# Kernel optimization log

Hardware: AMD Instinct MI355X
Metric: run time of the kernel (lower is better)

The kernel has to match this reference:

```python
import jax, jax.numpy as jnp
import numpy as np

C = 1.0        # curvature parameter (manifold curvature -1/C)
EPS = 1e-7


def expmap0_space(v, k):
    # v: [..., ds] spatial tangent vector at the hyperboloid origin (time comp 0)
    # returns ambient point [..., ds+1] = (sqrt(k)cosh(|v|/sqrt(k)), sqrt(k)sinh(|v|/sqrt(k)) v/|v|)
    sk = jnp.sqrt(k)
    n = jnp.maximum(jnp.linalg.norm(v, axis=-1, keepdims=True), EPS)
    t = sk * jnp.cosh(n / sk)
    s = sk * jnp.sinh(n / sk) * (v / n)
    return jnp.concatenate([t, s], axis=-1)


def logmap0_space(p, k):
    # p: [..., ds+1] hyperboloid point -> spatial tangent [..., ds] at origin
    sk = jnp.sqrt(k)
    t, s = p[..., :1], p[..., 1:]
    ns = jnp.maximum(jnp.linalg.norm(s, axis=-1, keepdims=True), EPS)
    d = sk * jnp.arccosh(jnp.maximum(t / sk, 1.0 + EPS))
    return d * (s / ns)


def setup_inputs() -> dict:
    key = jax.random.key(0)
    N, DS, E = 50000, 127, 800000
    ks = jax.random.split(key, 8)
    x = jax.random.normal(ks[0], (N, DS), dtype=jnp.float32) * 0.1
    edge_src = jax.random.randint(ks[1], (E,), 0, N)
    edge_dst = jax.random.randint(ks[2], (E,), 0, N)
    edge_weight = jax.random.uniform(ks[3], (E,), dtype=jnp.float32) / 16.0  # ~1/deg norm
    sc = 1.0 / np.sqrt(DS)
    W1 = jax.random.normal(ks[4], (DS, DS), dtype=jnp.float32) * sc
    b1 = jnp.zeros((DS,), dtype=jnp.float32)
    W2 = jax.random.normal(ks[5], (DS, DS), dtype=jnp.float32) * sc
    b2 = jnp.zeros((DS,), dtype=jnp.float32)
    return {"x": x, "W1": W1, "b1": b1, "W2": W2, "b2": b2,
            "edge_src": edge_src, "edge_dst": edge_dst, "edge_weight": edge_weight}


def reference(x, W1, b1, W2, b2, edge_src, edge_dst, edge_weight):
    N = x.shape[0]
    # encode(): cat zero time column + expmap0 onto hyperboloid
    p = expmap0_space(x, C)                 # [N, ds+1]
    h = logmap0_space(p, C)                 # tangent features at origin [N, ds]
    for (W, b) in ((W1, b1), (W2, b2)):
        # hyperbolic linear in tangent space
        z = h @ W + b                       # [N, ds]
        # adjacency-based neighbor aggregation (sparse spmm via edge list)
        msg = edge_weight[:, None] * z[edge_src]          # [E, ds] irregular gather
        agg = jax.ops.segment_sum(msg, edge_dst, num_segments=N)
        # activation + skip connection, back onto the manifold between layers
        h = jax.nn.relu(agg) + h
        h = logmap0_space(expmap0_space(h, C), C)
    return expmap0_space(h, C)              # [N, ds+1] on hyperboloid
```

## Files before the change

kernel.cpp:

```cpp
#include <hip/hip_runtime.h>

#define EPS 1e-7f
#define DS 127
#define DP 128
#define NBMAX 512
#define CAP 4096
#define CH 2048
#define PADB ((DP * DP + DP + 255) / 256)
#define BM 64

typedef short bf16x8 __attribute__((ext_vector_type(8)));
typedef float f32x4  __attribute__((ext_vector_type(4)));
typedef float f32x2  __attribute__((ext_vector_type(2)));

__device__ __forceinline__ float wave_sum(float v) {
#pragma unroll
    for (int off = 32; off > 0; off >>= 1)
        v += __shfl_xor(v, off, 64);
    return v;
}

__device__ __forceinline__ int wave_sum_i(int v) {
#pragma unroll
    for (int off = 32; off > 0; off >>= 1)
        v += __shfl_xor(v, off, 64);
    return v;
}

__device__ __forceinline__ unsigned short f2bf(float f) {
    unsigned u = __float_as_uint(f);
    unsigned r = (u + 0x7FFFu + ((u >> 16) & 1u)) >> 16;
    return (unsigned short)r;
}

__device__ __forceinline__ unsigned pack_bf2(float a, float b) {
    return (unsigned)f2bf(a) | ((unsigned)f2bf(b) << 16);
}

__device__ __forceinline__ unsigned char f2fp8(float v) {
    return (unsigned char)(__builtin_amdgcn_cvt_pk_fp8_f32(v, v, 0, false) & 0xFF);
}

__device__ __forceinline__ float logexp_scale(float n2) {
    float nrm = sqrtf(n2);
    return (nrm >= 4.472136e-4f) ? 1.0f : (4.472136e-4f / fmaxf(nrm, EPS));
}

__device__ __forceinline__ void sinhcosh(float n, float& sh, float& ch) {
    float e  = __expf(n);
    float em = __expf(-n);
    sh = 0.5f * (e - em);
    ch = 0.5f * (e + em);
}

__device__ __forceinline__ void padT_dev(int pb, int tid,
        const float* __restrict__ W, const float* __restrict__ b,
        unsigned short* __restrict__ Wt, float* __restrict__ bp) {
    int i = pb * 256 + tid;
    if (i < DP * DP) {
        int n = i >> 7, k = i & (DP - 1);
        Wt[i] = (k < DS && n < DS) ? f2bf(W[k * DS + n]) : (unsigned short)0;
    } else if (i < DP * DP + DP) {
        int j = i - DP * DP;
        bp[j] = (j < DS) ? b[j] : 0.f;
    }
}

__device__ void binA_dev(int abid, int tid,
        const int* __restrict__ es, const int* __restrict__ ed,
        const float* __restrict__ ew,
        int* __restrict__ gcnt, unsigned* __restrict__ stg_pk,
        unsigned char* __restrict__ stg_r, int E) {
    __shared__ int  lcnt[NBMAX];
    __shared__ int  loff[NBMAX];
    __shared__ int  gbase[NBMAX];
    __shared__ unsigned       lst_pk[CH];
    __shared__ unsigned short lst_d[CH];

    int lane = tid & 63;
    int base = abid * CH;
    int cnt  = min(CH, E - base);

    for (int b = tid; b < NBMAX; b += 256) lcnt[b] = 0;
    __syncthreads();

    unsigned pk[CH / 256];
    int      rd[CH / 256];
#pragma unroll
    for (int k = 0; k < CH / 256; k++) {
        int i = base + k * 256 + tid;
        if (i < E) {
            int d = ed[i];
            rd[k] = d;
            pk[k] = ((unsigned)f2bf(ew[i]) << 16) | (unsigned)es[i];
            atomicAdd(&lcnt[d >> 7], 1);
        } else {
            rd[k] = -1;
        }
    }
    __syncthreads();

    if (tid < 64) {
        int carry = 0;
        for (int c = 0; c < NBMAX; c += 64) {
            int v = lcnt[c + lane];
            int inc = v;
#pragma unroll
            for (int off = 1; off < 64; off <<= 1) {
                int t = __shfl_up(inc, off, 64);
                if (lane >= off) inc += t;
            }
            loff[c + lane] = carry + inc - v;
            carry += __shfl(inc, 63, 64);
        }
    }
    __syncthreads();
    for (int b = tid; b < NBMAX; b += 256) lcnt[b] = 0;
    __syncthreads();

#pragma unroll
    for (int k = 0; k < CH / 256; k++) {
        if (rd[k] >= 0) {
            int b = rd[k] >> 7;
            int slot = loff[b] + atomicAdd(&lcnt[b], 1);
            lst_pk[slot] = pk[k];
            lst_d[slot]  = (unsigned short)rd[k];
        }
    }
    __syncthreads();

    for (int b = tid; b < NBMAX; b += 256) {
        int c = lcnt[b];
        gbase[b] = c ? atomicAdd(&gcnt[b], c) : 0;
    }
    __syncthreads();

    for (int s = tid; s < cnt; s += 256) {
        unsigned p = lst_pk[s];
        int d = lst_d[s];
        int b = d >> 7;
        int idx = gbase[b] + (s - loff[b]);
        if (idx >= CAP) idx = CAP - 1;
        stg_pk[(size_t)b * CAP + idx] = p;
        stg_r [(size_t)b * CAP + idx] = (unsigned char)(d & 127);
    }
}

__device__ void binB_dev(int b, int tid,
        const unsigned* __restrict__ stg_pk, const unsigned char* __restrict__ stg_r,
        const int* __restrict__ gcnt,
        int* __restrict__ row_start, unsigned* __restrict__ epk,
        int N, int E) {
    __shared__ int rcnt[128];
    __shared__ int roff[128];
    __shared__ int sh_bb;

    int lane = tid & 63;
    int wave = tid >> 6;
    int cnt  = min(gcnt[b], CAP);
    const unsigned*      in_pk = stg_pk + (size_t)b * CAP;
    const unsigned char* in_r  = stg_r  + (size_t)b * CAP;

    if (tid < 128) rcnt[tid] = 0;
    if (b == 0 && tid == 0) row_start[N] = E;
    __syncthreads();

    if (wave == 3) {
        int acc = 0;
        for (int c = lane; c < b; c += 64) acc += min(gcnt[c], CAP);
        acc = wave_sum_i(acc);
        if (lane == 0) sh_bb = acc;
    } else {
        for (int i = tid; i < cnt; i += 192)
            atomicAdd(&rcnt[in_r[i]], 1);
    }
    __syncthreads();
    int bb = sh_bb;

    if (tid < 64) {
        int carry = 0;
        for (int c = 0; c < 128; c += 64) {
            int v = rcnt[c + lane];
            int inc = v;
#pragma unroll
            for (int off = 1; off < 64; off <<= 1) {
                int t = __shfl_up(inc, off, 64);
                if (lane >= off) inc += t;
            }
            roff[c + lane] = carry + inc - v;
            carry += __shfl(inc, 63, 64);
        }
    }
    __syncthreads();

    if (tid < 128) {
        int row = b * 128 + tid;
        if (row < N) row_start[row] = bb + roff[tid];
        rcnt[tid] = 0;
    }
    __syncthreads();

    for (int i = tid; i < cnt; i += 256) {
        int r = in_r[i];
        int pos = atomicAdd(&rcnt[r], 1);
        epk[bb + roff[r] + pos] = in_pk[i];
    }
}

__global__ __launch_bounds__(256) void k1_kernel(
        const int* __restrict__ es, const int* __restrict__ ed,
        const float* __restrict__ ew,
        int* __restrict__ gcnt, unsigned* __restrict__ stg_pk,
        unsigned char* __restrict__ stg_r, int E,
        const float* __restrict__ W1, const float* __restrict__ b1,
        unsigned short* __restrict__ Wt1, float* __restrict__ bp1,
        const float* __restrict__ W2, const float* __restrict__ b2,
        unsigned short* __restrict__ Wt2, float* __restrict__ bp2, int nA) {
    int bid = blockIdx.x;
    int tid = threadIdx.x;
    if (bid < nA) {
        binA_dev(bid, tid, es, ed, ew, gcnt, stg_pk, stg_r, E);
        return;
    }
    bid -= nA;
    int layer = (bid >= PADB);
    int pb    = bid - layer * PADB;
    padT_dev(pb, tid, layer ? W2 : W1, layer ? b2 : b1,
             layer ? Wt2 : Wt1, layer ? bp2 : bp1);
}

__device__ void fgemm_dev(int gbid, int tid,
        const float* __restrict__ x, unsigned* __restrict__ hbu,
        const unsigned short* __restrict__ Wt, const float* __restrict__ bp,
        unsigned char* __restrict__ z8, int N) {
    __shared__ unsigned sha[64 * 64];

    int wave = tid >> 6;
    int lane = tid & 63;
    int r0   = gbid * BM;

    f32x2 xv[16];
#pragma unroll
    for (int r = 0; r < 16; r++) {
        int row = r0 + wave * 16 + r;
        if (row < N) {
            const float* rp = x + (size_t)row * DS;
            xv[r].x = rp[2 * lane];
            xv[r].y = (lane < 63) ? rp[2 * lane + 1] : 0.f;
        } else {
            xv[r].x = 0.f; xv[r].y = 0.f;
        }
    }
#pragma unroll
    for (int r = 0; r < 16; r++) {
        int lr  = wave * 16 + r;
        int row = r0 + lr;
        float s = logexp_scale(wave_sum(xv[r].x * xv[r].x + xv[r].y * xv[r].y));
        unsigned pk = pack_bf2(s * xv[r].x, (lane < 63) ? s * xv[r].y : 0.f);
        sha[lr * 64 + lane] = pk;
        if (row < N) hbu[(size_t)row * (DP / 2) + lane] = pk;
    }

    int m    = lane & 15;
    int quad = lane >> 4;

    f32x4 acc[8];
#pragma unroll
    for (int t = 0; t < 8; t++) acc[t] = (f32x4){0.f, 0.f, 0.f, 0.f};

    const unsigned* shrow = sha + (size_t)(wave * 16 + m) * 64;
    bf16x8 a[4];
#pragma unroll
    for (int kq = 0; kq < 4; kq++)
        a[kq] = *(const bf16x8*)(shrow + kq * 16 + quad * 4);

#pragma unroll
    for (int kq = 0; kq < 4; kq++) {
#pragma unroll
        for (int nt = 0; nt < 8; nt++) {
            bf16x8 bfr = ((const bf16x8*)(Wt + (size_t)(nt * 16 + m) * DP))[kq * 4 + quad];
            acc[nt] = __builtin_amdgcn_mfma_f32_16x16x32_bf16(a[kq], bfr, acc[nt], 0, 0, 0);
        }
    }

    int rw0 = r0 + wave * 16;
#pragma unroll
    for (int nt = 0; nt < 8; nt++) {
        float bias = bp[nt * 16 + m];
#pragma unroll
        for (int reg = 0; reg < 4; reg++) {
            int row = rw0 + quad * 4 + reg;
            if (row < N)
                z8[(size_t)row * DP + nt * 16 + m] = f2fp8(acc[nt][reg] + bias);
        }
    }
}

__global__ __launch_bounds__(256) void k2_kernel(
        const unsigned* __restrict__ stg_pk, const unsigned char* __restrict__ stg_r,
        const int* __restrict__ gcnt,
        int* __restrict__ row_start, unsigned* __restrict__ epk,
        const float* __restrict__ x, unsigned* __restrict__ hbu,
        const unsigned short* __restrict__ Wt, const float* __restrict__ bp,
        unsigned char* __restrict__ z8, int N, int E, int nB) {
    int bid = blockIdx.x;
    int tid = threadIdx.x;
    if (bid < nB) {
        binB_dev(bid, tid, stg_pk, stg_r, gcnt, row_start, epk, N, E);
        return;
    }
    fgemm_dev(bid - nB, tid, x, hbu, Wt, bp, z8, N);
}

__global__ __launch_bounds__(256) void gemm_kernel(
        const unsigned short* __restrict__ hb,
        const unsigned short* __restrict__ Wt,
        const float* __restrict__ bp,
        unsigned char* __restrict__ z8, int N) {
    int wave = threadIdx.x >> 6;
    int lane = threadIdx.x & 63;
    int m    = lane & 15;
    int quad = lane >> 4;
    int r0   = blockIdx.x * BM + wave * 16;

    f32x4 acc[8];
#pragma unroll
    for (int t = 0; t < 8; t++) acc[t] = (f32x4){0.f, 0.f, 0.f, 0.f};

    const bf16x8* arow = (const bf16x8*)(hb + (size_t)(r0 + m) * DP);
    bf16x8 a[4];
#pragma unroll
    for (int kq = 0; kq < 4; kq++) a[kq] = arow[kq * 4 + quad];

#pragma unroll
    for (int kq = 0; kq < 4; kq++) {
#pragma unroll
        for (int nt = 0; nt < 8; nt++) {
            bf16x8 bfr = ((const bf16x8*)(Wt + (size_t)(nt * 16 + m) * DP))[kq * 4 + quad];
            acc[nt] = __builtin_amdgcn_mfma_f32_16x16x32_bf16(a[kq], bfr, acc[nt], 0, 0, 0);
        }
    }

#pragma unroll
    for (int nt = 0; nt < 8; nt++) {
        float bias = bp[nt * 16 + m];
#pragma unroll
        for (int reg = 0; reg < 4; reg++) {
            int row = r0 + quad * 4 + reg;
            if (row < N)
                z8[(size_t)row * DP + nt * 16 + m] = f2fp8(acc[nt][reg] + bias);
        }
    }
}

__device__ __forceinline__ void agg_round32(
        const unsigned char* __restrict__ zc, const unsigned* __restrict__ epk,
        int e, int end, bool lo, int q4, float* A) {
    unsigned p[32];
#pragma unroll
    for (int i = 0; i < 32; i++) {
        unsigned v = epk[e + i];
        p[i] = (e + i < end) ? v : 0u;
    }
    unsigned ud[16];
#pragma unroll
    for (int i = 0; i < 16; i++) {
        unsigned sel = lo ? p[2 * i] : p[2 * i + 1];
        ud[i] = *(const unsigned*)(zc + (((size_t)(sel & 0xFFFFu)) << 7) + q4);
    }
#pragma unroll
    for (int i = 0; i < 16; i++) {
        unsigned sel = lo ? p[2 * i] : p[2 * i + 1];
        float wf = __uint_as_float(sel & 0xFFFF0000u);
        f32x2 zl = __builtin_amdgcn_cvt_pk_f32_fp8(ud[i], false);
        f32x2 zh = __builtin_amdgcn_cvt_pk_f32_fp8(ud[i], true);
        A[0] = fmaf(wf, zl.x, A[0]);
        A[1] = fmaf(wf, zl.y, A[1]);
        A[2] = fmaf(wf, zh.x, A[2]);
        A[3] = fmaf(wf, zh.y, A[3]);
    }
}

__device__ __forceinline__ void agg_round32_pair(
        const unsigned char* __restrict__ zc, const unsigned* __restrict__ epk,
        int e0, int end0, int e1, int end1, bool lo, int q4,
        float* A, float* B) {
    unsigned p0[32], p1[32];
#pragma unroll
    for (int i = 0; i < 32; i++) {
        unsigned v = epk[e0 + i];
        p0[i] = (e0 + i < end0) ? v : 0u;
    }
#pragma unroll
    for (int i = 0; i < 32; i++) {
        unsigned v = epk[e1 + i];
        p1[i] = (e1 + i < end1) ? v : 0u;
    }
    unsigned ud0[16], ud1[16];
#pragma unroll
    for (int i = 0; i < 16; i++) {
        unsigned sel = lo ? p0[2 * i] : p0[2 * i + 1];
        ud0[i] = *(const unsigned*)(zc + (((size_t)(sel & 0xFFFFu)) << 7) + q4);
    }
#pragma unroll
    for (int i = 0; i < 16; i++) {
        unsigned sel = lo ? p1[2 * i] : p1[2 * i + 1];
        ud1[i] = *(const unsigned*)(zc + (((size_t)(sel & 0xFFFFu)) << 7) + q4);
    }
#pragma unroll
    for (int i = 0; i < 16; i++) {
        unsigned sel = lo ? p0[2 * i] : p0[2 * i + 1];
        float wf = __uint_as_float(sel & 0xFFFF0000u);
        f32x2 zl = __builtin_amdgcn_cvt_pk_f32_fp8(ud0[i], false);
        f32x2 zh = __builtin_amdgcn_cvt_pk_f32_fp8(ud0[i], true);
        A[0] = fmaf(wf, zl.x, A[0]);
        A[1] = fmaf(wf, zl.y, A[1]);
        A[2] = fmaf(wf, zh.x, A[2]);
        A[3] = fmaf(wf, zh.y, A[3]);
    }
#pragma unroll
    for (int i = 0; i < 16; i++) {
        unsigned sel = lo ? p1[2 * i] : p1[2 * i + 1];
        float wf = __uint_as_float(sel & 0xFFFF0000u);
        f32x2 zl = __builtin_amdgcn_cvt_pk_f32_fp8(ud1[i], false);
        f32x2 zh = __builtin_amdgcn_cvt_pk_f32_fp8(ud1[i], true);
        B[0] = fmaf(wf, zl.x, B[0]);
        B[1] = fmaf(wf, zl.y, B[1]);
        B[2] = fmaf(wf, zh.x, B[2]);
        B[3] = fmaf(wf, zh.y, B[3]);
    }
}

template <bool LAST>
__global__ __launch_bounds__(256) void agg_f_tpl(
                          const unsigned char* __restrict__ zc,
                          const unsigned* __restrict__ hbu_in,
                          const int* __restrict__ row_start,
                          const unsigned* __restrict__ epk,
                          unsigned* __restrict__ hbu_out,
                          float* __restrict__ out, int N) {
    int wid  = (int)((blockIdx.x * blockDim.x + threadIdx.x) >> 6);
    int lane = threadIdx.x & 63;
    int gw0  = wid * 2;
    if (gw0 >= N) return;
    gw0 = __builtin_amdgcn_readfirstlane(gw0);
    bool lo = (lane < 32);
    int  q  = lane & 31;
    int  q4 = q << 2;
    bool has1 = (gw0 + 1 < N);

    int rs0 = row_start[gw0];
    int rs1 = row_start[gw0 + 1];
    int rs2 = has1 ? row_start[gw0 + 2] : rs1;

    uint2 hu0 = *(const uint2*)(hbu_in + (size_t)gw0 * (DP / 2) + 2 * q);
    uint2 hu1 = has1 ? *(const uint2*)(hbu_in + (size_t)(gw0 + 1) * (DP / 2) + 2 * q)
                     : make_uint2(0u, 0u);

    float A[4] = {0.f, 0.f, 0.f, 0.f};
    float B[4] = {0.f, 0.f, 0.f, 0.f};

    agg_round32_pair(zc, epk, rs0, rs1, rs1, rs2, lo, q4, A, B);
    int e0 = rs0 + 32, e1 = rs1 + 32;
    while (e0 < rs1) { agg_round32(zc, epk, e0, rs1, lo, q4, A); e0 += 32; }
    while (e1 < rs2) { agg_round32(zc, epk, e1, rs2, lo, q4, B); e1 += 32; }

#pragma unroll
    for (int k = 0; k < 4; k++) {
        A[k] += __shfl_xor(A[k], 32, 64);
        B[k] += __shfl_xor(B[k], 32, 64);
    }

    unsigned hx[2][2] = {{hu0.x, hu0.y}, {hu1.x, hu1.y}};
#pragma unroll
    for (int r = 0; r < 2; r++) {
        if (r == 1 && !has1) break;
        int gw = gw0 + r;
        const float* Ac = (r == 0) ? A : B;
        float x0 = __uint_as_float(hx[r][0] << 16)          + fmaxf(Ac[0], 0.f);
        float x1 = __uint_as_float(hx[r][0] & 0xFFFF0000u)  + fmaxf(Ac[1], 0.f);
        float x2 = __uint_as_float(hx[r][1] << 16)          + fmaxf(Ac[2], 0.f);
        float x3 = __uint_as_float(hx[r][1] & 0xFFFF0000u)  + fmaxf(Ac[3], 0.f);

        float n2 = x0 * x0 + x1 * x1 + x2 * x2 + x3 * x3;
#pragma unroll
        for (int off = 16; off > 0; off >>= 1)
            n2 += __shfl_xor(n2, off, 64);

        float scale = logexp_scale(n2);
        float y0 = scale * x0, y1 = scale * x1;
        float y2 = scale * x2, y3 = scale * x3;

        if (!LAST) {
            unsigned* orow = hbu_out + (size_t)gw * (DP / 2);
            if (lo) orow[2 * q]     = pack_bf2(y0, y1);
            else    orow[2 * q + 1] = pack_bf2(y2, y3);
        } else {
            float ny = fmaxf(scale * sqrtf(n2), EPS);
            float shy, chy;
            sinhcosh(ny, shy, chy);
            float sc = shy / ny;
            float* orow = out + (size_t)gw * DP;
            if (lane == 0) orow[0] = chy;
            if (lo) {
                orow[1 + 4 * q] = sc * y0;
                orow[2 + 4 * q] = sc * y1;
            } else {
                orow[3 + 4 * q] = sc * y2;
                if (q < 31) orow[4 + 4 * q] = sc * y3;
            }
        }
    }
}

extern "C" void kernel_launch(void* const* d_in, const int* in_sizes, int n_in,
                              void* d_out, int out_size, void* d_ws, size_t ws_size,
                              hipStream_t stream) {
    const float* x  = (const float*)d_in[0];
    const float* W1 = (const float*)d_in[1];
    const float* b1 = (const float*)d_in[2];
    const float* W2 = (const float*)d_in[3];
    const float* b2 = (const float*)d_in[4];
    const int*   es = (const int*)d_in[5];
    const int*   ed = (const int*)d_in[6];
    const float* ew = (const float*)d_in[7];

    const int N  = in_sizes[0] / DS;
    const int E  = in_sizes[5];
    const int NR = (N + BM - 1) / BM * BM;
    const int NB = (N + 127) >> 7;

    unsigned short* hb  = (unsigned short*)d_ws;
    unsigned char*  z8  = (unsigned char*)(hb + (size_t)NR * DP);
    unsigned short* Wt1 = (unsigned short*)(z8 + (size_t)N * DP);
    unsigned short* Wt2 = Wt1 + DP * DP;
    float* bp1          = (float*)(Wt2 + DP * DP);
    float* bp2          = bp1 + DP;
    unsigned* epk       = (unsigned*)(bp2 + DP);
    int*   row_start    = (int*)(epk + E);
    int*   gcnt         = row_start + N + 1;
    unsigned* stg_pk    = (unsigned*)(gcnt + NBMAX);
    unsigned char* stg_r = (unsigned char*)(stg_pk + (size_t)NBMAX * CAP);

    unsigned* hbu = (unsigned*)hb;

    const int gemmBlocks = (N + BM - 1) / BM;
    const int binABlocks = (E + CH - 1) / CH;
    const int aggWaves   = (N + 1) / 2;
    const int aggBlocks  = (aggWaves + 3) / 4;

    hipMemsetAsync(gcnt, 0, NBMAX * sizeof(int), stream);

    k1_kernel<<<binABlocks + 2 * PADB, 256, 0, stream>>>(
        es, ed, ew, gcnt, stg_pk, stg_r, E,
        W1, b1, Wt1, bp1, W2, b2, Wt2, bp2, binABlocks);

    k2_kernel<<<NB + gemmBlocks, 256, 0, stream>>>(
        stg_pk, stg_r, gcnt, row_start, epk,
        x, hbu, Wt1, bp1, z8, N, E, NB);

    agg_f_tpl<false><<<aggBlocks, 256, 0, stream>>>(z8, hbu, row_start, epk,
                                                    hbu, nullptr, N);

    gemm_kernel<<<gemmBlocks, 256, 0, stream>>>(hb, Wt2, bp2, z8, N);

    agg_f_tpl<true><<<aggBlocks, 256, 0, stream>>>(z8, hbu, row_start, epk,
                                                   nullptr, (float*)d_out, N);
}
```

Before: 222.1 us.

## Make aggregation kernel persistent with grid-stride rows, one row per wave

Replaces the two-rows-per-wave aggregation with a persistent grid-stride loop. A fixed grid of 2048 blocks is launched with an occupancy hint of 8 blocks per CU, and each wave handles one destination row at a time. The bf16 output store is merged into a single 64-bit write from the lower half-wave, and the final fp32 row is likewise written only by the lower half. This cuts launch and tail imbalance and register pressure, at the cost of fewer independent gathers in flight per wave than the paired-row version had.

```diff
diff --git a/kernel.cpp b/kernel.cpp
--- a/kernel.cpp
+++ b/kernel.cpp
@@ -353,7 +353,7 @@
     }
 }
 
-__device__ __forceinline__ void agg_round32(
+__device__ __forceinline__ void agg_win32(
         const unsigned char* __restrict__ zc, const unsigned* __restrict__ epk,
         int e, int end, bool lo, int q4, float* A) {
     unsigned p[32];
@@ -381,106 +381,40 @@
     }
 }
 
-__device__ __forceinline__ void agg_round32_pair(
-        const unsigned char* __restrict__ zc, const unsigned* __restrict__ epk,
-        int e0, int end0, int e1, int end1, bool lo, int q4,
-        float* A, float* B) {
-    unsigned p0[32], p1[32];
-#pragma unroll
-    for (int i = 0; i < 32; i++) {
-        unsigned v = epk[e0 + i];
-        p0[i] = (e0 + i < end0) ? v : 0u;
-    }
-#pragma unroll
-    for (int i = 0; i < 32; i++) {
-        unsigned v = epk[e1 + i];
-        p1[i] = (e1 + i < end1) ? v : 0u;
-    }
-    unsigned ud0[16], ud1[16];
-#pragma unroll
-    for (int i = 0; i < 16; i++) {
-        unsigned sel = lo ? p0[2 * i] : p0[2 * i + 1];
-        ud0[i] = *(const unsigned*)(zc + (((size_t)(sel & 0xFFFFu)) << 7) + q4);
-    }
-#pragma unroll
-    for (int i = 0; i < 16; i++) {
-        unsigned sel = lo ? p1[2 * i] : p1[2 * i + 1];
-        ud1[i] = *(const unsigned*)(zc + (((size_t)(sel & 0xFFFFu)) << 7) + q4);
-    }
-#pragma unroll
-    for (int i = 0; i < 16; i++) {
-        unsigned sel = lo ? p0[2 * i] : p0[2 * i + 1];
-        float wf = __uint_as_float(sel & 0xFFFF0000u);
-        f32x2 zl = __builtin_amdgcn_cvt_pk_f32_fp8(ud0[i], false);
-        f32x2 zh = __builtin_amdgcn_cvt_pk_f32_fp8(ud0[i], true);
-        A[0] = fmaf(wf, zl.x, A[0]);
-        A[1] = fmaf(wf, zl.y, A[1]);
-        A[2] = fmaf(wf, zh.x, A[2]);
-        A[3] = fmaf(wf, zh.y, A[3]);
-    }
-#pragma unroll
-    for (int i = 0; i < 16; i++) {
-        unsigned sel = lo ? p1[2 * i] : p1[2 * i + 1];
-        float wf = __uint_as_float(sel & 0xFFFF0000u);
-        f32x2 zl = __builtin_amdgcn_cvt_pk_f32_fp8(ud1[i], false);
-        f32x2 zh = __builtin_amdgcn_cvt_pk_f32_fp8(ud1[i], true);
-        B[0] = fmaf(wf, zl.x, B[0]);
-        B[1] = fmaf(wf, zl.y, B[1]);
-        B[2] = fmaf(wf, zh.x, B[2]);
-        B[3] = fmaf(wf, zh.y, B[3]);
-    }
-}
-
 template <bool LAST>
-__global__ __launch_bounds__(256) void agg_f_tpl(
+__global__ __launch_bounds__(256, 8) void agg_f_tpl(
                           const unsigned char* __restrict__ zc,
                           const unsigned* __restrict__ hbu_in,
                           const int* __restrict__ row_start,
                           const unsigned* __restrict__ epk,
                           unsigned* __restrict__ hbu_out,
-                          float* __restrict__ out, int N) {
-    int wid  = (int)((blockIdx.x * blockDim.x + threadIdx.x) >> 6);
+                          float* __restrict__ out, int N, int W) {
+    int gwave = (int)((blockIdx.x * blockDim.x + threadIdx.x) >> 6);
+    gwave = __builtin_amdgcn_readfirstlane(gwave);
     int lane = threadIdx.x & 63;
-    int gw0  = wid * 2;
-    if (gw0 >= N) return;
-    gw0 = __builtin_amdgcn_readfirstlane(gw0);
     bool lo = (lane < 32);
     int  q  = lane & 31;
     int  q4 = q << 2;
-    bool has1 = (gw0 + 1 < N);
-
-    int rs0 = row_start[gw0];
-    int rs1 = row_start[gw0 + 1];
-    int rs2 = has1 ? row_start[gw0 + 2] : rs1;
-
-    uint2 hu0 = *(const uint2*)(hbu_in + (size_t)gw0 * (DP / 2) + 2 * q);
-    uint2 hu1 = has1 ? *(const uint2*)(hbu_in + (size_t)(gw0 + 1) * (DP / 2) + 2 * q)
-                     : make_uint2(0u, 0u);
-
-    float A[4] = {0.f, 0.f, 0.f, 0.f};
-    float B[4] = {0.f, 0.f, 0.f, 0.f};
-
-    agg_round32_pair(zc, epk, rs0, rs1, rs1, rs2, lo, q4, A, B);
-    int e0 = rs0 + 32, e1 = rs1 + 32;
-    while (e0 < rs1) { agg_round32(zc, epk, e0, rs1, lo, q4, A); e0 += 32; }
-    while (e1 < rs2) { agg_round32(zc, epk, e1, rs2, lo, q4, B); e1 += 32; }
-
-#pragma unroll
-    for (int k = 0; k < 4; k++) {
-        A[k] += __shfl_xor(A[k], 32, 64);
-        B[k] += __shfl_xor(B[k], 32, 64);
-    }
-
-    unsigned hx[2][2] = {{hu0.x, hu0.y}, {hu1.x, hu1.y}};
-#pragma unroll
-    for (int r = 0; r < 2; r++) {
-        if (r == 1 && !has1) break;
-        int gw = gw0 + r;
-        const float* Ac = (r == 0) ? A : B;
-        float x0 = __uint_as_float(hx[r][0] << 16)          + fmaxf(Ac[0], 0.f);
-        float x1 = __uint_as_float(hx[r][0] & 0xFFFF0000u)  + fmaxf(Ac[1], 0.f);
-        float x2 = __uint_as_float(hx[r][1] << 16)          + fmaxf(Ac[2], 0.f);
-        float x3 = __uint_as_float(hx[r][1] & 0xFFFF0000u)  + fmaxf(Ac[3], 0.f);
+
+    for (int r = gwave; r < N; r += W) {
+        int rs0 = row_start[r];
+        int rs1 = row_start[r + 1];
+
+        uint2 hu = *(const uint2*)(hbu_in + (size_t)r * (DP / 2) + 2 * q);
+
+        float A[4] = {0.f, 0.f, 0.f, 0.f};
+        agg_win32(zc, epk, rs0, rs1, lo, q4, A);
+        for (int e = rs0 + 32; e < rs1; e += 32)
+            agg_win32(zc, epk, e, rs1, lo, q4, A);
+
+#pragma unroll
+        for (int k = 0; k < 4; k++)
+            A[k] += __shfl_xor(A[k], 32, 64);
+
+        float x0 = __uint_as_float(hu.x << 16)         + fmaxf(A[0], 0.f);
+        float x1 = __uint_as_float(hu.x & 0xFFFF0000u) + fmaxf(A[1], 0.f);
+        float x2 = __uint_as_float(hu.y << 16)         + fmaxf(A[2], 0.f);
+        float x3 = __uint_as_float(hu.y & 0xFFFF0000u) + fmaxf(A[3], 0.f);
 
         float n2 = x0 * x0 + x1 * x1 + x2 * x2 + x3 * x3;
 #pragma unroll
@@ -492,20 +426,20 @@
         float y2 = scale * x2, y3 = scale * x3;
 
         if (!LAST) {
-            unsigned* orow = hbu_out + (size_t)gw * (DP / 2);
-            if (lo) orow[2 * q]     = pack_bf2(y0, y1);
-            else    orow[2 * q + 1] = pack_bf2(y2, y3);
+            if (lo) {
+                uint2 st = make_uint2(pack_bf2(y0, y1), pack_bf2(y2, y3));
+                *(uint2*)(hbu_out + (size_t)r * (DP / 2) + 2 * q) = st;
+            }
         } else {
             float ny = fmaxf(scale * sqrtf(n2), EPS);
             float shy, chy;
             sinhcosh(ny, shy, chy);
             float sc = shy / ny;
-            float* orow = out + (size_t)gw * DP;
+            float* orow = out + (size_t)r * DP;
             if (lane == 0) orow[0] = chy;
             if (lo) {
                 orow[1 + 4 * q] = sc * y0;
                 orow[2 + 4 * q] = sc * y1;
-            } else {
                 orow[3 + 4 * q] = sc * y2;
                 if (q < 31) orow[4 + 4 * q] = sc * y3;
             }
@@ -546,8 +480,8 @@
 
     const int gemmBlocks = (N + BM - 1) / BM;
     const int binABlocks = (E + CH - 1) / CH;
-    const int aggWaves   = (N + 1) / 2;
-    const int aggBlocks  = (aggWaves + 3) / 4;
+    const int aggBlocks  = 2048;
+    const int aggWavesW  = aggBlocks * 4;
 
     hipMemsetAsync(gcnt, 0, NBMAX * sizeof(int), stream);
 
@@ -560,10 +494,10 @@
         x, hbu, Wt1, bp1, z8, N, E, NB);
 
     agg_f_tpl<false><<<aggBlocks, 256, 0, stream>>>(z8, hbu, row_start, epk,
-                                                    hbu, nullptr, N);
+                                                    hbu, nullptr, N, aggWavesW);
 
     gemm_kernel<<<gemmBlocks, 256, 0, stream>>>(hb, Wt2, bp2, z8, N);
 
     agg_f_tpl<true><<<aggBlocks, 256, 0, stream>>>(z8, hbu, row_start, epk,
-                                                   nullptr, (float*)d_out, N);
-}
+                                                   nullptr, (float*)d_out, N, aggWavesW);
+}
```

After: 231.0 us. 1.04x slower.
